# Performance work log

Hardware: AMD Instinct MI355X
Metric: run time of the kernel (lower is better)

The kernel has to match this reference:

```python
import jax, jax.numpy as jnp
import numpy as np

B, C, N_ANGLES, N_POS, IMG = 16, 1, 360, 512, 512


def setup_inputs() -> dict:
    key = jax.random.key(0)
    sinogram = jax.random.normal(key, (B, C, N_ANGLES, N_POS), dtype=jnp.float32)
    # uniform angles over [0, pi) and a centered detector grid in pixel units
    thetas = (jnp.arange(N_ANGLES, dtype=jnp.float32) * (np.pi / N_ANGLES))
    positions = jnp.arange(N_POS, dtype=jnp.float32) - (N_POS - 1) / 2.0
    return {"sinogram": sinogram, "thetas": thetas, "positions": positions, "image_size": IMG}


def _backproject(sinogram, thetas, positions, image_size):
    """Radon backprojection: out[b,c,y,x] = sum_a lininterp(sino[b,c,a,:], t(x,y,a))."""
    Bn, Cn, A, P = sinogram.shape
    xs = jnp.arange(image_size, dtype=jnp.float32) - (image_size - 1) / 2.0
    X, Y = jnp.meshgrid(xs, xs, indexing="xy")  # [H, W], image-centered coords
    pos0 = positions[0]
    dp = positions[1] - positions[0]  # uniform detector spacing assumed

    sino_a = jnp.moveaxis(sinogram, 2, 0)  # [A, B, C, P]

    def body(acc, inp):
        theta, s = inp  # theta scalar, s: [B, C, P]
        t = X * jnp.cos(theta) + Y * jnp.sin(theta)          # [H, W] ray coordinate
        fidx = (t - pos0) / dp                                # fractional detector index
        i0f = jnp.floor(fidx)
        w = fidx - i0f                                        # interpolation weight
        i0 = i0f.astype(jnp.int32)
        i1 = i0 + 1
        v0 = ((i0 >= 0) & (i0 < P)).astype(jnp.float32)       # zero outside detector
        v1 = ((i1 >= 0) & (i1 < P)).astype(jnp.float32)
        i0c = jnp.clip(i0, 0, P - 1)
        i1c = jnp.clip(i1, 0, P - 1)
        g0 = s[:, :, i0c]                                     # gather -> [B, C, H, W]
        g1 = s[:, :, i1c]
        contrib = (1.0 - w) * v0 * g0 + w * v1 * g1
        return acc + contrib, None

    acc0 = jnp.zeros((Bn, Cn, image_size, image_size), dtype=sinogram.dtype)
    out, _ = jax.lax.scan(body, acc0, (thetas, sino_a))
    return out


def reference(sinogram, thetas, positions, image_size):
    return _backproject(sinogram, thetas, positions, image_size)
```

## Files before the change

### kernel.cpp

```cpp
#include <hip/hip_runtime.h>
#include <math.h>

#define NA 360
#define NP 512
#define NB 16
#define IMG 512
#define PS 514
#define ACH 8
#define NCH (NA / ACH)
#define NPT 32

typedef unsigned int uint32;
typedef __fp16 half2 __attribute__((ext_vector_type(2)));

static __device__ __forceinline__ half2 u2h(uint32 u) {
    union { uint32 u; half2 h; } v; v.u = u; return v.h;
}
static __device__ __forceinline__ uint32 pk(float a, float b) {
    union { half2 h; uint32 u; } v;
    v.h = __builtin_amdgcn_cvt_pkrtz(a, b);
    return v.u;
}

#if __has_builtin(__builtin_amdgcn_fdot2)
static __device__ __forceinline__ float dot2(half2 w, half2 v, float acc) {
    return __builtin_amdgcn_fdot2(w, v, acc, false);
}
#else
static __device__ __forceinline__ float dot2(half2 w, half2 v, float acc) {
    return fmaf((float)w.x, (float)v.x, fmaf((float)w.y, (float)v.y, acc));
}
#endif

static __device__ __forceinline__ void write_tab(const float* thetas,
                                                 const float* positions,
                                                 float4* tab, int a) {
    double th = (double)thetas[a];
    double p0 = (double)positions[0];
    double dp = (double)positions[1] - p0;
    double c = cos(th) / dp, s = sin(th) / dp;
    tab[a] = make_float4((float)c, (float)s, (float)(-p0 / dp),
                         (float)((fabs(c) + fabs(s)) * 7.5));
}

__global__ void stage(const float* __restrict__ sino,
                      const float* __restrict__ thetas,
                      const float* __restrict__ positions,
                      float4* __restrict__ tab,
                      uint4* __restrict__ st) {
    if (blockIdx.x == gridDim.x - 1) {
        int a = threadIdx.x;
        if (a < NA) write_tab(thetas, positions, tab, a);
        int a2 = threadIdx.x + 256;
        if (a2 < NA) write_tab(thetas, positions, tab, a2);
        return;
    }
    int idx = blockIdx.x * 256 + threadIdx.x;
    if (idx >= NA * PS) return;
    int a  = idx / PS;
    int pp = idx - a * PS;
    int p0 = pp - 1;
    uint32 r[16];
#pragma unroll
    for (int b = 0; b < NB; ++b) {
        const float* row = sino + ((size_t)b * NA + a) * NP;
        float f0 = (p0 >= 0 && p0 < NP) ? row[p0] : 0.0f;
        float f1 = (pp < NP) ? row[pp] : 0.0f;
        r[b] = pk(f0, f1);
    }
#pragma unroll
    for (int k = 0; k < 4; ++k)
        st[(size_t)k * (NA * PS) + idx] =
            make_uint4(r[4 * k], r[4 * k + 1], r[4 * k + 2], r[4 * k + 3]);
}

static __device__ __forceinline__ int pmin_of(float tc, float tw) {
    float fmn = fminf(fmaxf(tc - tw, -1.0f), 512.0f);
    return min(max((int)floorf(fmn) - 1, 0), PS - NPT);
}

__launch_bounds__(256)
__global__ void backproject(const uint4* __restrict__ st,
                            const float4* __restrict__ tab,
                            float* __restrict__ out) {
    __shared__ uint4 buf[2][ACH * 4 * NPT];
    __shared__ int pm_lds[NA];
    const int tid = threadIdx.y * 16 + threadIdx.x;
    const int x = blockIdx.x * 16 + threadIdx.x;
    const int y = blockIdx.y * 16 + threadIdx.y;
    const float xs = (float)x - 255.5f;
    const float ys = (float)y - 255.5f;
    const float xc = (float)(blockIdx.x * 16) + 7.5f - 255.5f;
    const float yc = (float)(blockIdx.y * 16) + 7.5f - 255.5f;

    for (int a = tid; a < NA; a += 256) {
        const float4 t = tab[a];
        float tc = fmaf(xc, t.x, fmaf(yc, t.y, t.z));
        pm_lds[a] = pmin_of(tc, t.w);
    }
    __syncthreads();

    float acc[NB];
#pragma unroll
    for (int b = 0; b < NB; ++b) acc[b] = 0.0f;

    const int qld = (tid >> 5) & 3;
    const int ptl = tid & 31;
    const int hl  = tid >> 7;

    auto issue = [&](int ch, int bsel) {
#pragma unroll
        for (int j = 0; j < 4; ++j) {
            const int a = ch * ACH + 2 * j + hl;
            const int pm = pm_lds[a];
            const uint4* gp = &st[(size_t)qld * (NA * PS) + (size_t)a * PS + pm + ptl];
            uint4* lp = &buf[bsel][tid + 256 * j];
            __builtin_amdgcn_global_load_lds(
                (__attribute__((address_space(1))) const void*)gp,
                (__attribute__((address_space(3))) void*)lp, 16, 0, 0);
        }
    };

    issue(0, 0);

#pragma unroll 1
    for (int ch = 0; ch < NCH; ++ch) {
        __syncthreads();
        if (ch + 1 < NCH) issue(ch + 1, (ch + 1) & 1);

        const int a0 = ch * ACH;
        const uint4* b = buf[ch & 1];
#pragma unroll
        for (int al = 0; al < ACH; ++al) {
            const float4 t = tab[a0 + al];
            float fidx = fmaf(xs, t.x, fmaf(ys, t.y, t.z));
            fidx = fminf(fmaxf(fidx, -1.0f), 512.0f);
            const float fl = floorf(fidx);
            const float w = fidx - fl;
            const half2 wp = u2h(pk(1.0f - w, w));
            const int idx = ((int)fl + 1) - pm_lds[a0 + al];
            const uint4 d0 = b[al * 128 + 0 * 32 + idx];
            const uint4 d1 = b[al * 128 + 1 * 32 + idx];
            const uint4 d2 = b[al * 128 + 2 * 32 + idx];
            const uint4 d3 = b[al * 128 + 3 * 32 + idx];
            acc[0]  = dot2(wp, u2h(d0.x), acc[0]);
            acc[1]  = dot2(wp, u2h(d0.y), acc[1]);
            acc[2]  = dot2(wp, u2h(d0.z), acc[2]);
            acc[3]  = dot2(wp, u2h(d0.w), acc[3]);
            acc[4]  = dot2(wp, u2h(d1.x), acc[4]);
            acc[5]  = dot2(wp, u2h(d1.y), acc[5]);
            acc[6]  = dot2(wp, u2h(d1.z), acc[6]);
            acc[7]  = dot2(wp, u2h(d1.w), acc[7]);
            acc[8]  = dot2(wp, u2h(d2.x), acc[8]);
            acc[9]  = dot2(wp, u2h(d2.y), acc[9]);
            acc[10] = dot2(wp, u2h(d2.z), acc[10]);
            acc[11] = dot2(wp, u2h(d2.w), acc[11]);
            acc[12] = dot2(wp, u2h(d3.x), acc[12]);
            acc[13] = dot2(wp, u2h(d3.y), acc[13]);
            acc[14] = dot2(wp, u2h(d3.z), acc[14]);
            acc[15] = dot2(wp, u2h(d3.w), acc[15]);
        }
    }

    const size_t pix = (size_t)y * IMG + x;
#pragma unroll
    for (int b = 0; b < NB; ++b)
        out[(size_t)b * (IMG * IMG) + pix] = acc[b];
}

extern "C" void kernel_launch(void* const* d_in, const int* in_sizes, int n_in,
                              void* d_out, int out_size, void* d_ws, size_t ws_size,
                              hipStream_t stream) {
    const float* sino      = (const float*)d_in[0];
    const float* thetas    = (const float*)d_in[1];
    const float* positions = (const float*)d_in[2];
    float* out = (float*)d_out;

    float4* tab = (float4*)d_ws;
    uint4*  st  = (uint4*)((char*)d_ws + 8192);

    const int nb = (NA * PS + 255) / 256 + 1;
    stage<<<dim3(nb), dim3(256), 0, stream>>>(sino, thetas, positions, tab, st);
    backproject<<<dim3(IMG / 16, IMG / 16), dim3(16, 16), 0, stream>>>(st, tab, out);
}
```

Before: 168.3 us.

## Split sinogram reads between LDS staging and direct per-thread global gathers

The backprojection kernel now stages only batch planes 0-1 through the LDS DMA double buffer. Planes 2-3 are fetched with per-pixel global loads that are software-pipelined two angles ahead. This halves LDS footprint and LDS read traffic, spreading load across the L1/L2 path and LDS. The stage kernel also gets 4x more threads, each writing one uint4, for better parallelism. The risk is scattered global gathers with extra latency and register pressure.

Result: slower. 196.9 us (+17.0%).

```diff
diff --git a/kernel.cpp b/kernel.cpp
--- a/kernel.cpp
+++ b/kernel.cpp
@@ -56,22 +56,21 @@
         return;
     }
     int idx = blockIdx.x * 256 + threadIdx.x;
-    if (idx >= NA * PS) return;
-    int a  = idx / PS;
-    int pp = idx - a * PS;
-    int p0 = pp - 1;
-    uint32 r[16];
-#pragma unroll
-    for (int b = 0; b < NB; ++b) {
-        const float* row = sino + ((size_t)b * NA + a) * NP;
+    if (idx >= 4 * NA * PS) return;
+    const int k   = idx / (NA * PS);
+    const int rem = idx - k * (NA * PS);
+    const int a   = rem / PS;
+    const int pp  = rem - a * PS;
+    const int p0  = pp - 1;
+    uint32 r[4];
+#pragma unroll
+    for (int i = 0; i < 4; ++i) {
+        const float* row = sino + ((size_t)(4 * k + i) * NA + a) * NP;
         float f0 = (p0 >= 0 && p0 < NP) ? row[p0] : 0.0f;
         float f1 = (pp < NP) ? row[pp] : 0.0f;
-        r[b] = pk(f0, f1);
-    }
-#pragma unroll
-    for (int k = 0; k < 4; ++k)
-        st[(size_t)k * (NA * PS) + idx] =
-            make_uint4(r[4 * k], r[4 * k + 1], r[4 * k + 2], r[4 * k + 3]);
+        r[i] = pk(f0, f1);
+    }
+    st[idx] = make_uint4(r[0], r[1], r[2], r[3]);
 }
 
 static __device__ __forceinline__ int pmin_of(float tc, float tw) {
@@ -83,7 +82,7 @@
 __global__ void backproject(const uint4* __restrict__ st,
                             const float4* __restrict__ tab,
                             float* __restrict__ out) {
-    __shared__ uint4 buf[2][ACH * 4 * NPT];
+    __shared__ uint4 buf[2][ACH * 2 * NPT];
     __shared__ int pm_lds[NA];
     const int tid = threadIdx.y * 16 + threadIdx.x;
     const int x = blockIdx.x * 16 + threadIdx.x;
@@ -104,61 +103,107 @@
 #pragma unroll
     for (int b = 0; b < NB; ++b) acc[b] = 0.0f;
 
-    const int qld = (tid >> 5) & 3;
-    const int ptl = tid & 31;
-    const int hl  = tid >> 7;
-
-    auto issue = [&](int ch, int bsel) {
-#pragma unroll
-        for (int j = 0; j < 4; ++j) {
-            const int a = ch * ACH + 2 * j + hl;
+    const uint4* __restrict__ pl2 = st + (size_t)2 * (NA * PS);
+    const uint4* __restrict__ pl3 = st + (size_t)3 * (NA * PS);
+
+    auto issue_dma = [&](int ch, int bsel) {
+#pragma unroll
+        for (int j = 0; j < 2; ++j) {
+            const int s  = tid + 256 * j;
+            const int al = s >> 6, q = (s >> 5) & 1, pt = s & 31;
+            const int a  = ch * ACH + al;
             const int pm = pm_lds[a];
-            const uint4* gp = &st[(size_t)qld * (NA * PS) + (size_t)a * PS + pm + ptl];
-            uint4* lp = &buf[bsel][tid + 256 * j];
+            const uint4* gp = &st[(size_t)q * (NA * PS) + (size_t)a * PS + pm + pt];
             __builtin_amdgcn_global_load_lds(
                 (__attribute__((address_space(1))) const void*)gp,
-                (__attribute__((address_space(3))) void*)lp, 16, 0, 0);
+                (__attribute__((address_space(3))) void*)&buf[bsel][s], 16, 0, 0);
         }
     };
 
-    issue(0, 0);
+    auto gidx = [&](int a) -> int {
+        const float4 t = tab[a];
+        float fidx = fmaf(xs, t.x, fmaf(ys, t.y, t.z));
+        fidx = fminf(fmaxf(fidx, -1.0f), 512.0f);
+        return a * PS + ((int)floorf(fidx) + 1);
+    };
+
+    issue_dma(0, 0);
+    int iA = gidx(0);
+    uint4 gA2 = pl2[iA], gA3 = pl3[iA];
+    int iB = gidx(1);
+    uint4 gB2 = pl2[iB], gB3 = pl3[iB];
 
 #pragma unroll 1
     for (int ch = 0; ch < NCH; ++ch) {
         __syncthreads();
-        if (ch + 1 < NCH) issue(ch + 1, (ch + 1) & 1);
+        if (ch + 1 < NCH) issue_dma(ch + 1, (ch + 1) & 1);
 
         const int a0 = ch * ACH;
         const uint4* b = buf[ch & 1];
 #pragma unroll
-        for (int al = 0; al < ACH; ++al) {
-            const float4 t = tab[a0 + al];
-            float fidx = fmaf(xs, t.x, fmaf(ys, t.y, t.z));
-            fidx = fminf(fmaxf(fidx, -1.0f), 512.0f);
-            const float fl = floorf(fidx);
-            const float w = fidx - fl;
-            const half2 wp = u2h(pk(1.0f - w, w));
-            const int idx = ((int)fl + 1) - pm_lds[a0 + al];
-            const uint4 d0 = b[al * 128 + 0 * 32 + idx];
-            const uint4 d1 = b[al * 128 + 1 * 32 + idx];
-            const uint4 d2 = b[al * 128 + 2 * 32 + idx];
-            const uint4 d3 = b[al * 128 + 3 * 32 + idx];
-            acc[0]  = dot2(wp, u2h(d0.x), acc[0]);
-            acc[1]  = dot2(wp, u2h(d0.y), acc[1]);
-            acc[2]  = dot2(wp, u2h(d0.z), acc[2]);
-            acc[3]  = dot2(wp, u2h(d0.w), acc[3]);
-            acc[4]  = dot2(wp, u2h(d1.x), acc[4]);
-            acc[5]  = dot2(wp, u2h(d1.y), acc[5]);
-            acc[6]  = dot2(wp, u2h(d1.z), acc[6]);
-            acc[7]  = dot2(wp, u2h(d1.w), acc[7]);
-            acc[8]  = dot2(wp, u2h(d2.x), acc[8]);
-            acc[9]  = dot2(wp, u2h(d2.y), acc[9]);
-            acc[10] = dot2(wp, u2h(d2.z), acc[10]);
-            acc[11] = dot2(wp, u2h(d2.w), acc[11]);
-            acc[12] = dot2(wp, u2h(d3.x), acc[12]);
-            acc[13] = dot2(wp, u2h(d3.y), acc[13]);
-            acc[14] = dot2(wp, u2h(d3.z), acc[14]);
-            acc[15] = dot2(wp, u2h(d3.w), acc[15]);
+        for (int half = 0; half < ACH / 2; ++half) {
+            {
+                const int a = a0 + 2 * half;
+                const float4 t = tab[a];
+                float fidx = fmaf(xs, t.x, fmaf(ys, t.y, t.z));
+                fidx = fminf(fmaxf(fidx, -1.0f), 512.0f);
+                const float fl = floorf(fidx);
+                const float w = fidx - fl;
+                const half2 wp = u2h(pk(1.0f - w, w));
+                const int idx = ((int)fl + 1) - pm_lds[a];
+                const uint4 d0 = b[(2 * half) * 64 + idx];
+                const uint4 d1 = b[(2 * half) * 64 + 32 + idx];
+                acc[0]  = dot2(wp, u2h(d0.x), acc[0]);
+                acc[1]  = dot2(wp, u2h(d0.y), acc[1]);
+                acc[2]  = dot2(wp, u2h(d0.z), acc[2]);
+                acc[3]  = dot2(wp, u2h(d0.w), acc[3]);
+                acc[4]  = dot2(wp, u2h(d1.x), acc[4]);
+                acc[5]  = dot2(wp, u2h(d1.y), acc[5]);
+                acc[6]  = dot2(wp, u2h(d1.z), acc[6]);
+                acc[7]  = dot2(wp, u2h(d1.w), acc[7]);
+                acc[8]  = dot2(wp, u2h(gA2.x), acc[8]);
+                acc[9]  = dot2(wp, u2h(gA2.y), acc[9]);
+                acc[10] = dot2(wp, u2h(gA2.z), acc[10]);
+                acc[11] = dot2(wp, u2h(gA2.w), acc[11]);
+                acc[12] = dot2(wp, u2h(gA3.x), acc[12]);
+                acc[13] = dot2(wp, u2h(gA3.y), acc[13]);
+                acc[14] = dot2(wp, u2h(gA3.z), acc[14]);
+                acc[15] = dot2(wp, u2h(gA3.w), acc[15]);
+                const int an = min(a + 2, NA - 1);
+                const int i2 = gidx(an);
+                gA2 = pl2[i2]; gA3 = pl3[i2];
+            }
+            {
+                const int a = a0 + 2 * half + 1;
+                const float4 t = tab[a];
+                float fidx = fmaf(xs, t.x, fmaf(ys, t.y, t.z));
+                fidx = fminf(fmaxf(fidx, -1.0f), 512.0f);
+                const float fl = floorf(fidx);
+                const float w = fidx - fl;
+                const half2 wp = u2h(pk(1.0f - w, w));
+                const int idx = ((int)fl + 1) - pm_lds[a];
+                const uint4 d0 = b[(2 * half + 1) * 64 + idx];
+                const uint4 d1 = b[(2 * half + 1) * 64 + 32 + idx];
+                acc[0]  = dot2(wp, u2h(d0.x), acc[0]);
+                acc[1]  = dot2(wp, u2h(d0.y), acc[1]);
+                acc[2]  = dot2(wp, u2h(d0.z), acc[2]);
+                acc[3]  = dot2(wp, u2h(d0.w), acc[3]);
+                acc[4]  = dot2(wp, u2h(d1.x), acc[4]);
+                acc[5]  = dot2(wp, u2h(d1.y), acc[5]);
+                acc[6]  = dot2(wp, u2h(d1.z), acc[6]);
+                acc[7]  = dot2(wp, u2h(d1.w), acc[7]);
+                acc[8]  = dot2(wp, u2h(gB2.x), acc[8]);
+                acc[9]  = dot2(wp, u2h(gB2.y), acc[9]);
+                acc[10] = dot2(wp, u2h(gB2.z), acc[10]);
+                acc[11] = dot2(wp, u2h(gB2.w), acc[11]);
+                acc[12] = dot2(wp, u2h(gB3.x), acc[12]);
+                acc[13] = dot2(wp, u2h(gB3.y), acc[13]);
+                acc[14] = dot2(wp, u2h(gB3.z), acc[14]);
+                acc[15] = dot2(wp, u2h(gB3.w), acc[15]);
+                const int an = min(a + 2, NA - 1);
+                const int i2 = gidx(an);
+                gB2 = pl2[i2]; gB3 = pl3[i2];
+            }
         }
     }
 
@@ -179,7 +224,7 @@
     float4* tab = (float4*)d_ws;
     uint4*  st  = (uint4*)((char*)d_ws + 8192);
 
-    const int nb = (NA * PS + 255) / 256 + 1;
+    const int nb = (4 * NA * PS + 255) / 256 + 1;
     stage<<<dim3(nb), dim3(256), 0, stream>>>(sino, thetas, positions, tab, st);
     backproject<<<dim3(IMG / 16, IMG / 16), dim3(16, 16), 0, stream>>>(st, tab, out);
 }
```
